# Kernel tuning notes

Hardware: AMD Instinct MI355X
Metric: run time of the kernel (lower is better)

## Reference

```python
import jax, jax.numpy as jnp
import numpy as np

EMBED = 1024
HEADS = 16
HEAD_DIM = EMBED // HEADS
T = 1024
B = 2
TEMP = 1.0
EPS = 1e-20


def setup_inputs() -> dict:
    key = jax.random.key(0)
    ks = jax.random.split(key, 8)
    s = 0.02  # xavier-ish init scale
    return {
        "g": jax.random.normal(ks[0], (T, B, EMBED), dtype=jnp.float32),
        "h": jax.random.normal(ks[1], (T, B, EMBED), dtype=jnp.float32),
        "g_in_w": jax.random.normal(ks[2], (3 * EMBED, EMBED), dtype=jnp.float32) * s,
        "g_in_b": jnp.zeros((3 * EMBED,), dtype=jnp.float32),
        "h_in_w": jax.random.normal(ks[3], (2 * EMBED, EMBED), dtype=jnp.float32) * s,
        "h_in_b": jnp.zeros((2 * EMBED,), dtype=jnp.float32),
        "g_out_w": jax.random.normal(ks[4], (EMBED, EMBED), dtype=jnp.float32) * s,
        "g_out_b": jnp.zeros((EMBED,), dtype=jnp.float32),
        "h_out_w": jax.random.normal(ks[5], (EMBED, EMBED), dtype=jnp.float32) * s,
        "h_out_b": jnp.zeros((EMBED,), dtype=jnp.float32),
    }


def reference(g, h, g_in_w, g_in_b, h_in_w, h_in_b, g_out_w, g_out_b, h_out_w, h_out_b):
    Tt, Bb, E = g.shape
    H, d = HEADS, HEAD_DIM

    # fused qkv projection on g stream, kv on h stream (F.linear: x @ W^T + b)
    q, gk, gv = jnp.split(g @ g_in_w.T + g_in_b, 3, axis=-1)
    hk, hv = jnp.split(h @ h_in_w.T + h_in_b, 2, axis=-1)
    q = q * (d ** -0.5)

    def to_heads(x):  # [T,B,E] -> [B,H,T,d]
        return x.reshape(Tt, Bb, H, d).transpose(1, 2, 0, 3)

    q, gk, gv, hk, hv = map(to_heads, (q, gk, gv, hk, hv))

    # dual-stream attention scores
    g_scores = jnp.einsum("bhtd,bhsd->bhts", q, gk)
    h_scores = jnp.einsum("bhtd,bhsd->bhts", q, hk)

    g_p = jax.nn.softmax(g_scores, axis=-1)
    h_p = jax.nn.softmax(h_scores, axis=-1)

    # gumbel-softmax sample of h_scores (mode='gumbel', temperature=TEMP)
    u = jax.random.uniform(jax.random.key(42), h_scores.shape, dtype=h_scores.dtype)
    noise = -jnp.log(-jnp.log(u + EPS) + EPS)
    sample = jax.nn.softmax((jax.nn.log_softmax(h_scores, axis=-1) + noise) / TEMP, axis=-1)

    g_attn = jnp.einsum("bhts,bhsd->bhtd", g_p, gv)
    h_attn = jnp.einsum("bhts,bhsd->bhtd", sample, hv)

    def merge(x):  # [B,H,T,d] -> [T,B,E]
        return x.transpose(2, 0, 1, 3).reshape(Tt, Bb, E)

    g_out = merge(g_attn) @ g_out_w.T + g_out_b
    h_out = merge(h_attn) @ h_out_w.T + h_out_b
    return g_out, h_out
```

## Files before the change

### kernel.cpp

```cpp
#include <hip/hip_runtime.h>
#include <stdint.h>

#define T_SEQ 1024

typedef __attribute__((ext_vector_type(8))) short short8;
typedef __attribute__((ext_vector_type(4))) float f32x4;
typedef __attribute__((ext_vector_type(4))) unsigned short ushort4v;
typedef __attribute__((ext_vector_type(8))) unsigned short ushort8v;

__device__ __forceinline__ unsigned short f2bf(float f) {
  union { float f; uint32_t u; } v; v.f = f;
  return (unsigned short)((v.u + 0x7fffu + ((v.u >> 16) & 1u)) >> 16);
}
__device__ __forceinline__ float bf2f(unsigned short u) {
  union { uint32_t u; float f; } v; v.u = ((uint32_t)u) << 16;
  return v.f;
}

__device__ __forceinline__ uint32_t tf_bits(uint32_t flat) {
  const uint32_t ks1 = 42u;
  const uint32_t ks2 = 0x1BD11BDAu ^ 42u;
  uint32_t x0 = 0u;
  uint32_t x1 = flat + ks1;
#define TFR(r) { x0 += x1; x1 = (x1 << (r)) | (x1 >> (32 - (r))); x1 ^= x0; }
  TFR(13) TFR(15) TFR(26) TFR(6)
  x0 += ks1; x1 += ks2 + 1u;
  TFR(17) TFR(29) TFR(16) TFR(24)
  x0 += ks2; x1 += 2u;
  TFR(13) TFR(15) TFR(26) TFR(6)
  x1 += ks1 + 3u;
  TFR(17) TFR(29) TFR(16) TFR(24)
  x0 += ks1; x1 += ks2 + 4u;
  TFR(13) TFR(15) TFR(26) TFR(6)
  x0 += ks2; x1 += 5u;
#undef TFR
  return x0 ^ x1;
}

__device__ __forceinline__ float gumbel_noise(uint32_t flat) {
  const uint32_t bits = tf_bits(flat);
  const float u = __uint_as_float((bits >> 9) | 0x3f800000u) - 1.0f;
  return -__logf(-__logf(u + 1e-20f) + 1e-20f);
}

__global__ __launch_bounds__(256) void convert_pre(
    const float* __restrict__ g, const float* __restrict__ h,
    const float* __restrict__ wgi_f, const float* __restrict__ whi_f,
    const float* __restrict__ wgo_f, const float* __restrict__ who_f,
    unsigned short* __restrict__ ghi, unsigned short* __restrict__ glo,
    unsigned short* __restrict__ hhi, unsigned short* __restrict__ hlo,
    unsigned short* __restrict__ wgi, unsigned short* __restrict__ whi,
    unsigned short* __restrict__ wgo, unsigned short* __restrict__ who)
{
  const int64_t Q_SPLIT = 1048576;
  const int64_t Q_TOTAL = Q_SPLIT + 1835008;
  for (int64_t qd = (int64_t)blockIdx.x * 256 + threadIdx.x; qd < Q_TOTAL;
       qd += (int64_t)gridDim.x * 256) {
    if (qd < Q_SPLIT) {
      const int which = qd >= 524288;
      const int64_t e = (qd - (which ? 524288 : 0)) * 4;
      const float4 v = *(const float4*)((which ? h : g) + e);
      ushort4v hi = {f2bf(v.x), f2bf(v.y), f2bf(v.z), f2bf(v.w)};
      ushort4v lo = {f2bf(v.x - bf2f(hi[0])), f2bf(v.y - bf2f(hi[1])),
                     f2bf(v.z - bf2f(hi[2])), f2bf(v.w - bf2f(hi[3]))};
      *(ushort4v*)((which ? hhi : ghi) + e) = hi;
      *(ushort4v*)((which ? hlo : glo) + e) = lo;
    } else {
      int64_t off = qd - Q_SPLIT;
      const float* src; unsigned short* dst;
      if (off < 786432)                 { src = wgi_f; dst = wgi; }
      else if (off < 1310720)           { off -= 786432;  src = whi_f; dst = whi; }
      else if (off < 1572864)           { off -= 1310720; src = wgo_f; dst = wgo; }
      else                              { off -= 1572864; src = who_f; dst = who; }
      const int64_t e = off * 4;
      const float4 v = *(const float4*)(src + e);
      ushort4v u = {f2bf(v.x), f2bf(v.y), f2bf(v.z), f2bf(v.w)};
      *(ushort4v*)(dst + e) = u;
    }
  }
}

template<bool SPLIT, bool BF16OUT>
__device__ __forceinline__ void gemm_bf16_core(
    const unsigned short* __restrict__ Ahi_g, const unsigned short* __restrict__ Alo_g,
    const unsigned short* __restrict__ Wg_, const float* __restrict__ bias,
    int N, int K, int m0, int n0, int scale_limit, void* Cout,
    unsigned short* sA, unsigned short* sL, unsigned short* sW)
{
  const int tid = threadIdx.x;
  const int srow = tid >> 1;
  const int scol = (tid & 1) << 5;
  const int w = tid >> 6;
  const int wr = (w >> 1) << 6, wc = (w & 1) << 6;
  const int lane = tid & 63;
  const int txl = lane & 15, q = lane >> 4;

  f32x4 acc[4][4];
#pragma unroll
  for (int i = 0; i < 4; i++)
#pragma unroll
    for (int j = 0; j < 4; j++) acc[i][j] = (f32x4){0.f, 0.f, 0.f, 0.f};

  for (int k0 = 0; k0 < K; k0 += 64) {
    const unsigned short* Ap = Ahi_g + (size_t)(m0 + srow) * K + k0 + scol;
    const unsigned short* Lp = Alo_g + (size_t)(m0 + srow) * K + k0 + scol;
    const unsigned short* Wp = Wg_  + (size_t)(n0 + srow) * K + k0 + scol;
    ushort8v a8[4], l8[4], w8[4];
#pragma unroll
    for (int e = 0; e < 4; e++) {
      a8[e] = *(const ushort8v*)(Ap + 8 * e);
      if (SPLIT) l8[e] = *(const ushort8v*)(Lp + 8 * e);
      w8[e] = *(const ushort8v*)(Wp + 8 * e);
    }
    __syncthreads();
#pragma unroll
    for (int e = 0; e < 4; e++) {
      *(ushort8v*)&sA[srow * 72 + scol + 8 * e] = a8[e];
      if (SPLIT) *(ushort8v*)&sL[srow * 72 + scol + 8 * e] = l8[e];
      *(ushort8v*)&sW[srow * 72 + scol + 8 * e] = w8[e];
    }
    __syncthreads();
#pragma unroll
    for (int kk = 0; kk < 2; kk++) {
      short8 af[4], al[4], wf[4];
#pragma unroll
      for (int i = 0; i < 4; i++) {
        af[i] = *(const short8*)&sA[(wr + 16 * i + txl) * 72 + 32 * kk + 8 * q];
        if (SPLIT) al[i] = *(const short8*)&sL[(wr + 16 * i + txl) * 72 + 32 * kk + 8 * q];
      }
#pragma unroll
      for (int j = 0; j < 4; j++)
        wf[j] = *(const short8*)&sW[(wc + 16 * j + txl) * 72 + 32 * kk + 8 * q];
#pragma unroll
      for (int i = 0; i < 4; i++)
#pragma unroll
        for (int j = 0; j < 4; j++) {
          acc[i][j] = __builtin_amdgcn_mfma_f32_16x16x32_bf16(af[i], wf[j], acc[i][j], 0, 0, 0);
          if (SPLIT)
            acc[i][j] = __builtin_amdgcn_mfma_f32_16x16x32_bf16(al[i], wf[j], acc[i][j], 0, 0, 0);
        }
    }
  }

#pragma unroll
  for (int j = 0; j < 4; j++) {
    const int col = n0 + wc + 16 * j + txl;
    const float bj = bias[col];
    const float sc = (col < scale_limit) ? 0.125f : 1.0f;
#pragma unroll
    for (int i = 0; i < 4; i++) {
      const int rbase = m0 + wr + 16 * i + 4 * q;
#pragma unroll
      for (int r = 0; r < 4; r++) {
        const float v = (acc[i][j][r] + bj) * sc;
        if (BF16OUT) ((unsigned short*)Cout)[(size_t)(rbase + r) * N + col] = f2bf(v);
        else         ((float*)Cout)[(size_t)(rbase + r) * N + col] = v;
      }
    }
  }
}

__global__ __launch_bounds__(256, 2) void gemm_inproj(
    const unsigned short* __restrict__ ghi, const unsigned short* __restrict__ glo,
    const unsigned short* __restrict__ wgi, const float* __restrict__ bgi,
    const unsigned short* __restrict__ hhi, const unsigned short* __restrict__ hlo,
    const unsigned short* __restrict__ whi, const float* __restrict__ bhi,
    unsigned short* __restrict__ qkv, unsigned short* __restrict__ hkv)
{
  __shared__ __align__(16) unsigned short sm[27648];
  const int bx = blockIdx.x;
  const int m0 = blockIdx.y * 128;
  if (bx < 24)
    gemm_bf16_core<true, true>(ghi, glo, wgi, bgi, 3072, 1024, m0, bx * 128, 1024,
                               qkv, sm, sm + 9216, sm + 18432);
  else
    gemm_bf16_core<true, true>(hhi, hlo, whi, bhi, 2048, 1024, m0, (bx - 24) * 128, 0,
                               hkv, sm, sm + 9216, sm + 18432);
}

__global__ __launch_bounds__(256, 2) void gemm_outproj(
    const unsigned short* __restrict__ attnb,
    const unsigned short* __restrict__ wgo, const float* __restrict__ bgo,
    const unsigned short* __restrict__ who, const float* __restrict__ bho,
    float* __restrict__ out)
{
  __shared__ __align__(16) unsigned short sm[18432];
  const int m0 = blockIdx.y * 128;
  const unsigned short* Wp = (m0 < 2048) ? wgo : who;
  const float* bp = (m0 < 2048) ? bgo : bho;
  gemm_bf16_core<false, false>(attnb, attnb, Wp, bp, 1024, 1024, m0, blockIdx.x * 128, 0,
                               out, sm, sm, sm + 9216);
}

__global__ __launch_bounds__(256, 4) void attn_mfma(
    const unsigned short* __restrict__ qkv, const unsigned short* __restrict__ hkv,
    unsigned short* __restrict__ og, unsigned short* __restrict__ oh)
{
  __shared__ __align__(16) unsigned short smem[18432];
  unsigned short* KV = smem;
  unsigned short* PC = smem + 9216;
  unsigned short* QS = smem + 9216;

  const int tid = threadIdx.x;
  const int w = tid >> 6;
  const int lane = tid & 63;
  const int txl = lane & 15, q = lane >> 4;
  const int t0 = blockIdx.x * 64;
  const int bh = blockIdx.y;
  const int b = bh >> 4;
  const int hoff = (bh & 15) * 64;
  const int sr = tid >> 2;
  const int sc = (tid & 3) << 4;

  {
    const size_t gq = ((size_t)(t0 + sr) * 2 + b) * 3072 + hoff + sc;
    *(ushort8v*)&QS[sr * 72 + sc]     = *(const ushort8v*)&qkv[gq];
    *(ushort8v*)&QS[sr * 72 + sc + 8] = *(const ushort8v*)&qkv[gq + 8];
  }
  __syncthreads();
  const short8 aq0 = *(const short8*)&QS[(16 * w + txl) * 72 + 8 * q];
  const short8 aq1 = *(const short8*)&QS[(16 * w + txl) * 72 + 32 + 8 * q];

  f32x4 Og[4], Oh[4];
  float l_g[4], l_h[4];
#pragma unroll
  for (int i = 0; i < 4; i++) {
    Og[i] = (f32x4){0.f, 0.f, 0.f, 0.f};
    Oh[i] = (f32x4){0.f, 0.f, 0.f, 0.f};
    l_g[i] = 0.f; l_h[i] = 0.f;
  }

  unsigned short* pcg = PC + (w * 2 + 0) * 1152;
  unsigned short* pch = PC + (w * 2 + 1) * 1152;

  for (int s0 = 0; s0 < T_SEQ; s0 += 64) {
    __syncthreads();
    {
      const size_t grow = (size_t)(s0 + sr) * 2 + b;
      const ushort8v kg0 = *(const ushort8v*)&qkv[grow * 3072 + 1024 + hoff + sc];
      const ushort8v kg1 = *(const ushort8v*)&qkv[grow * 3072 + 1024 + hoff + sc + 8];
      const ushort8v kh0 = *(const ushort8v*)&hkv[grow * 2048 + hoff + sc];
      const ushort8v kh1 = *(const ushort8v*)&hkv[grow * 2048 + hoff + sc + 8];
      *(ushort8v*)&KV[sr * 72 + sc]            = kg0;
      *(ushort8v*)&KV[sr * 72 + sc + 8]        = kg1;
      *(ushort8v*)&KV[4608 + sr * 72 + sc]     = kh0;
      *(ushort8v*)&KV[4608 + sr * 72 + sc + 8] = kh1;
    }
    __syncthreads();

    f32x4 Sg[4], Sh[4];
    const f32x4 zz = (f32x4){0.f, 0.f, 0.f, 0.f};
#pragma unroll
    for (int nt = 0; nt < 4; nt++) {
      const int srw = (16 * nt + txl) * 72;
      const short8 bg0 = *(const short8*)&KV[srw + 8 * q];
      const short8 bg1 = *(const short8*)&KV[srw + 32 + 8 * q];
      const short8 bh0 = *(const short8*)&KV[4608 + srw + 8 * q];
      const short8 bh1 = *(const short8*)&KV[4608 + srw + 32 + 8 * q];
      f32x4 ag = __builtin_amdgcn_mfma_f32_16x16x32_bf16(aq0, bg0, zz, 0, 0, 0);
      ag = __builtin_amdgcn_mfma_f32_16x16x32_bf16(aq1, bg1, ag, 0, 0, 0);
      f32x4 ah = __builtin_amdgcn_mfma_f32_16x16x32_bf16(aq0, bh0, zz, 0, 0, 0);
      ah = __builtin_amdgcn_mfma_f32_16x16x32_bf16(aq1, bh1, ah, 0, 0, 0);
      Sg[nt] = ag; Sh[nt] = ah;
    }

#pragma unroll
    for (int nt = 0; nt < 4; nt++)
#pragma unroll
      for (int r = 0; r < 4; r++) {
        const uint32_t trow = (uint32_t)(t0 + 16 * w + 4 * q + r);
        const uint32_t scol_ = (uint32_t)(s0 + 16 * nt + txl);
        Sh[nt][r] += gumbel_noise(((uint32_t)bh << 20) | (trow << 10) | scol_);
      }

#pragma unroll
    for (int nt = 0; nt < 4; nt++) {
      float eg[4], eh[4];
#pragma unroll
      for (int r = 0; r < 4; r++) {
        eg[r] = __expf(Sg[nt][r]); l_g[r] += eg[r];
        eh[r] = __expf(Sh[nt][r]); l_h[r] += eh[r];
      }
      const int sbase = (16 * nt + txl) * 18 + 4 * q;
      *(uint32_t*)&pcg[sbase]     = (uint32_t)f2bf(eg[0]) | ((uint32_t)f2bf(eg[1]) << 16);
      *(uint32_t*)&pcg[sbase + 2] = (uint32_t)f2bf(eg[2]) | ((uint32_t)f2bf(eg[3]) << 16);
      *(uint32_t*)&pch[sbase]     = (uint32_t)f2bf(eh[0]) | ((uint32_t)f2bf(eh[1]) << 16);
      *(uint32_t*)&pch[sbase + 2] = (uint32_t)f2bf(eh[2]) | ((uint32_t)f2bf(eh[3]) << 16);
    }

    __syncthreads();
    {
      const int dd = tid >> 2;
      const int sseg = (tid & 3) * 16;
      ushort8v vg[2], vh[2];
#pragma unroll
      for (int p = 0; p < 2; p++)
#pragma unroll
        for (int m = 0; m < 8; m++) {
          const int s = sseg + 8 * p + m;
          const size_t grow = (size_t)(s0 + s) * 2 + b;
          vg[p][m] = qkv[grow * 3072 + 2048 + hoff + dd];
          vh[p][m] = hkv[grow * 2048 + 1024 + hoff + dd];
        }
#pragma unroll
      for (int p = 0; p < 2; p++) {
        *(ushort8v*)&KV[dd * 72 + sseg + 8 * p]        = vg[p];
        *(ushort8v*)&KV[4608 + dd * 72 + sseg + 8 * p] = vh[p];
      }
    }
    __syncthreads();

#pragma unroll
    for (int c = 0; c < 2; c++) {
      short8 apg, aph;
#pragma unroll
      for (int j = 0; j < 8; j++) {
        apg[j] = (short)pcg[(32 * c + 8 * q + j) * 18 + txl];
        aph[j] = (short)pch[(32 * c + 8 * q + j) * 18 + txl];
      }
#pragma unroll
      for (int nt = 0; nt < 4; nt++) {
        const int drow = (16 * nt + txl) * 72;
        const short8 bvg = *(const short8*)&KV[drow + 32 * c + 8 * q];
        const short8 bvh = *(const short8*)&KV[4608 + drow + 32 * c + 8 * q];
        Og[nt] = __builtin_amdgcn_mfma_f32_16x16x32_bf16(apg, bvg, Og[nt], 0, 0, 0);
        Oh[nt] = __builtin_amdgcn_mfma_f32_16x16x32_bf16(aph, bvh, Oh[nt], 0, 0, 0);
      }
    }
  }

#pragma unroll
  for (int r = 0; r < 4; r++) {
    float lg = l_g[r], lh = l_h[r];
    lg += __shfl_xor(lg, 1); lg += __shfl_xor(lg, 2);
    lg += __shfl_xor(lg, 4); lg += __shfl_xor(lg, 8);
    lh += __shfl_xor(lh, 1); lh += __shfl_xor(lh, 2);
    lh += __shfl_xor(lh, 4); lh += __shfl_xor(lh, 8);
    const float ig = 1.f / lg;
    const float ih = 1.f / lh;
    const size_t base = ((size_t)(t0 + 16 * w + 4 * q + r) * 2 + b) * 1024 + hoff;
#pragma unroll
    for (int nt = 0; nt < 4; nt++) {
      og[base + 16 * nt + txl] = f2bf(Og[nt][r] * ig);
      oh[base + 16 * nt + txl] = f2bf(Oh[nt][r] * ih);
    }
  }
}

extern "C" void kernel_launch(void* const* d_in, const int* in_sizes, int n_in,
                              void* d_out, int out_size, void* d_ws, size_t ws_size,
                              hipStream_t stream) {
  const float* g       = (const float*)d_in[0];
  const float* h       = (const float*)d_in[1];
  const float* g_in_w  = (const float*)d_in[2];
  const float* g_in_b  = (const float*)d_in[3];
  const float* h_in_w  = (const float*)d_in[4];
  const float* h_in_b  = (const float*)d_in[5];
  const float* g_out_w = (const float*)d_in[6];
  const float* g_out_b = (const float*)d_in[7];
  const float* h_out_w = (const float*)d_in[8];
  const float* h_out_b = (const float*)d_in[9];
  float* out = (float*)d_out;

  unsigned short* ws = (unsigned short*)d_ws;
  unsigned short* qkv   = ws;
  unsigned short* hkv   = qkv + (size_t)2048*3072;
  unsigned short* attnb = hkv + (size_t)2048*2048;
  unsigned short* ghi   = attnb + (size_t)4096*1024;
  unsigned short* glo   = ghi + (size_t)2048*1024;
  unsigned short* hhi   = glo + (size_t)2048*1024;
  unsigned short* hlo   = hhi + (size_t)2048*1024;
  unsigned short* wgi   = hlo + (size_t)2048*1024;
  unsigned short* whi   = wgi + (size_t)3072*1024;
  unsigned short* wgo   = whi + (size_t)2048*1024;
  unsigned short* who   = wgo + (size_t)1024*1024;

  convert_pre<<<1024, 256, 0, stream>>>(g, h, g_in_w, h_in_w, g_out_w, h_out_w,
                                        ghi, glo, hhi, hlo, wgi, whi, wgo, who);
  gemm_inproj<<<dim3(40, 16), 256, 0, stream>>>(
      ghi, glo, wgi, g_in_b, hhi, hlo, whi, h_in_b, qkv, hkv);
  attn_mfma<<<dim3(T_SEQ / 64, 32), 256, 0, stream>>>(
      qkv, hkv, attnb, attnb + (size_t)2048 * 1024);
  gemm_outproj<<<dim3(8, 32), 256, 0, stream>>>(
      attnb, wgo, g_out_b, who, h_out_b, out);
}
```

Baseline: 333.4 us.

## Split attention over two key-sequence halves and merge partial results in a new kernel

The attention kernel now takes a third grid dimension that splits the key/value sequence into two halves. Each half writes unnormalized fp32 partial outputs and per-head row sums to scratch, and a new merge kernel adds them, normalizes and converts to bf16. The goal is to double the number of attention blocks so the GPU's compute units are better filled. The cost is extra fp32 partial-result traffic, one more kernel launch, and scratch that now reuses the input-conversion buffers.

```diff
diff --git a/kernel.cpp b/kernel.cpp
--- a/kernel.cpp
+++ b/kernel.cpp
@@ -194,7 +194,7 @@
 
 __global__ __launch_bounds__(256, 4) void attn_mfma(
     const unsigned short* __restrict__ qkv, const unsigned short* __restrict__ hkv,
-    unsigned short* __restrict__ og, unsigned short* __restrict__ oh)
+    float* __restrict__ Opart, float* __restrict__ lpart)
 {
   __shared__ __align__(16) unsigned short smem[18432];
   unsigned short* KV = smem;
@@ -207,8 +207,10 @@
   const int txl = lane & 15, q = lane >> 4;
   const int t0 = blockIdx.x * 64;
   const int bh = blockIdx.y;
+  const int z = blockIdx.z;
   const int b = bh >> 4;
-  const int hoff = (bh & 15) * 64;
+  const int head = bh & 15;
+  const int hoff = head * 64;
   const int sr = tid >> 2;
   const int sc = (tid & 3) << 4;
 
@@ -233,7 +235,9 @@
   unsigned short* pcg = PC + (w * 2 + 0) * 1152;
   unsigned short* pch = PC + (w * 2 + 1) * 1152;
 
-  for (int s0 = 0; s0 < T_SEQ; s0 += 64) {
+  const int s_begin = z * (T_SEQ / 2);
+  const int s_end = s_begin + (T_SEQ / 2);
+  for (int s0 = s_begin; s0 < s_end; s0 += 64) {
     __syncthreads();
     {
       const size_t grow = (size_t)(s0 + sr) * 2 + b;
@@ -329,6 +333,10 @@
     }
   }
 
+  float* opg = Opart + ((size_t)(z * 2 + 0) * 2048) * 1024;
+  float* oph = Opart + ((size_t)(z * 2 + 1) * 2048) * 1024;
+  float* lpg = lpart + (size_t)(z * 2 + 0) * 2048 * 16;
+  float* lph = lpart + (size_t)(z * 2 + 1) * 2048 * 16;
 #pragma unroll
   for (int r = 0; r < 4; r++) {
     float lg = l_g[r], lh = l_h[r];
@@ -336,15 +344,38 @@
     lg += __shfl_xor(lg, 4); lg += __shfl_xor(lg, 8);
     lh += __shfl_xor(lh, 1); lh += __shfl_xor(lh, 2);
     lh += __shfl_xor(lh, 4); lh += __shfl_xor(lh, 8);
-    const float ig = 1.f / lg;
-    const float ih = 1.f / lh;
-    const size_t base = ((size_t)(t0 + 16 * w + 4 * q + r) * 2 + b) * 1024 + hoff;
+    const int row = (t0 + 16 * w + 4 * q + r) * 2 + b;
+    if (txl == 0) {
+      lpg[row * 16 + head] = lg;
+      lph[row * 16 + head] = lh;
+    }
+    const size_t base = (size_t)row * 1024 + hoff;
 #pragma unroll
     for (int nt = 0; nt < 4; nt++) {
-      og[base + 16 * nt + txl] = f2bf(Og[nt][r] * ig);
-      oh[base + 16 * nt + txl] = f2bf(Oh[nt][r] * ih);
-    }
-  }
+      opg[base + 16 * nt + txl] = Og[nt][r];
+      oph[base + 16 * nt + txl] = Oh[nt][r];
+    }
+  }
+}
+
+__global__ __launch_bounds__(256) void merge_attn(
+    const float* __restrict__ Opart, const float* __restrict__ lpart,
+    unsigned short* __restrict__ attnb)
+{
+  const int idx = blockIdx.x * 256 + threadIdx.x;
+  const int st = idx >> 19;
+  const int i = idx & 0x7FFFF;
+  const int row = i >> 8;
+  const int colq = i & 255;
+  const int head = colq >> 4;
+  const float4 o0 = *(const float4*)&Opart[((size_t)(0 + st) * 2048 + row) * 1024 + colq * 4];
+  const float4 o1 = *(const float4*)&Opart[((size_t)(2 + st) * 2048 + row) * 1024 + colq * 4];
+  const float l0 = lpart[(size_t)(0 + st) * 32768 + row * 16 + head];
+  const float l1 = lpart[(size_t)(2 + st) * 32768 + row * 16 + head];
+  const float inv = 1.0f / (l0 + l1);
+  ushort4v u = {f2bf((o0.x + o1.x) * inv), f2bf((o0.y + o1.y) * inv),
+                f2bf((o0.z + o1.z) * inv), f2bf((o0.w + o1.w) * inv)};
+  *(ushort4v*)&attnb[((size_t)st * 2048 + row) * 1024 + colq * 4] = u;
 }
 
 extern "C" void kernel_launch(void* const* d_in, const int* in_sizes, int n_in,
@@ -366,21 +397,24 @@
   unsigned short* qkv   = ws;
   unsigned short* hkv   = qkv + (size_t)2048*3072;
   unsigned short* attnb = hkv + (size_t)2048*2048;
-  unsigned short* ghi   = attnb + (size_t)4096*1024;
-  unsigned short* glo   = ghi + (size_t)2048*1024;
-  unsigned short* hhi   = glo + (size_t)2048*1024;
-  unsigned short* hlo   = hhi + (size_t)2048*1024;
-  unsigned short* wgi   = hlo + (size_t)2048*1024;
-  unsigned short* whi   = wgi + (size_t)3072*1024;
-  unsigned short* wgo   = whi + (size_t)2048*1024;
+  unsigned short* wgo   = attnb + (size_t)4096*1024;
   unsigned short* who   = wgo + (size_t)1024*1024;
+  unsigned short* scratch = who + (size_t)1024*1024;
+  unsigned short* ghi = scratch;
+  unsigned short* glo = ghi + (size_t)2048*1024;
+  unsigned short* hhi = glo + (size_t)2048*1024;
+  unsigned short* hlo = hhi + (size_t)2048*1024;
+  unsigned short* wgi = hlo + (size_t)2048*1024;
+  unsigned short* whi = wgi + (size_t)3072*1024;
+  float* Opart = (float*)scratch;
+  float* lpart = Opart + (size_t)4*2048*1024;
 
   convert_pre<<<1024, 256, 0, stream>>>(g, h, g_in_w, h_in_w, g_out_w, h_out_w,
                                         ghi, glo, hhi, hlo, wgi, whi, wgo, who);
   gemm_inproj<<<dim3(40, 16), 256, 0, stream>>>(
       ghi, glo, wgi, g_in_b, hhi, hlo, whi, h_in_b, qkv, hkv);
-  attn_mfma<<<dim3(T_SEQ / 64, 32), 256, 0, stream>>>(
-      qkv, hkv, attnb, attnb + (size_t)2048 * 1024);
+  attn_mfma<<<dim3(T_SEQ / 64, 32, 2), 256, 0, stream>>>(qkv, hkv, Opart, lpart);
+  merge_attn<<<4096, 256, 0, stream>>>(Opart, lpart, attnb);
   gemm_outproj<<<dim3(8, 32), 256, 0, stream>>>(
       attnb, wgo, g_out_b, who, h_out_b, out);
 }
```

Result: faster. 322.5 us (-3.3%).
